# Optimization experiments

Measured on AMD Instinct MI355X. Metric: run time of the kernel, lower is better.

## Reference

```python
import jax, jax.numpy as jnp
import numpy as np

DIM = 2048
N_HEADS = 32
N_KV_HEADS = 8
HEAD_DIM = 64
BATCH = 2
SEQ = 2048
N_REP = N_HEADS // N_KV_HEADS
SCALE = HEAD_DIM ** -0.5
ROPE_BASE = 10000.0


def setup_inputs() -> dict:
    key = jax.random.key(0)
    ks = jax.random.split(key, 5)
    x = jax.random.normal(ks[0], (BATCH, SEQ, DIM), dtype=jnp.float32)
    # weights stored as (in, out) so projection is x @ W
    Wq = jax.random.normal(ks[1], (DIM, N_HEADS * HEAD_DIM), dtype=jnp.float32) * (DIM ** -0.5)
    Wk = jax.random.normal(ks[2], (DIM, N_KV_HEADS * HEAD_DIM), dtype=jnp.float32) * (DIM ** -0.5)
    Wv = jax.random.normal(ks[3], (DIM, N_KV_HEADS * HEAD_DIM), dtype=jnp.float32) * (DIM ** -0.5)
    Wo = jax.random.normal(ks[4], (N_HEADS * HEAD_DIM, DIM), dtype=jnp.float32) * ((N_HEADS * HEAD_DIM) ** -0.5)
    # RoPE tables (seq, head_dim)
    inv_freq = 1.0 / (ROPE_BASE ** (jnp.arange(0, HEAD_DIM, 2, dtype=jnp.float32) / HEAD_DIM))
    t = jnp.arange(SEQ, dtype=jnp.float32)
    freqs = jnp.outer(t, inv_freq)                      # (S, D/2)
    emb = jnp.concatenate([freqs, freqs], axis=-1)      # (S, D)
    cos = jnp.cos(emb)
    sin = jnp.sin(emb)
    # additive causal mask (1,1,S,S)
    neg = jnp.finfo(jnp.float32).min
    causal = jnp.tril(jnp.ones((SEQ, SEQ), dtype=bool))
    attention_mask = jnp.where(causal, 0.0, neg)[None, None, :, :].astype(jnp.float32)
    return {"x": x, "Wq": Wq, "Wk": Wk, "Wv": Wv, "Wo": Wo,
            "cos": cos, "sin": sin, "attention_mask": attention_mask}


def _rotate_half(u):
    h = u.shape[-1] // 2
    return jnp.concatenate([-u[..., h:], u[..., :h]], axis=-1)


def reference(x, Wq, Wk, Wv, Wo, cos, sin, attention_mask):
    b, s, _ = x.shape
    q = (x @ Wq).reshape(b, s, N_HEADS, HEAD_DIM)
    k = (x @ Wk).reshape(b, s, N_KV_HEADS, HEAD_DIM)
    v = (x @ Wv).reshape(b, s, N_KV_HEADS, HEAD_DIM)
    # RoPE, broadcast over head dim (unsqueeze_dim=2)
    c = cos[None, :, None, :]
    sn = sin[None, :, None, :]
    q = q * c + _rotate_half(q) * sn
    k = k * c + _rotate_half(k) * sn
    # repeat KV heads for GQA: (b,s,kvh,d) -> (b,s,h,d)
    k = jnp.repeat(k, N_REP, axis=2)
    v = jnp.repeat(v, N_REP, axis=2)
    # (b,h,s,d)
    q = q.transpose(0, 2, 1, 3)
    k = k.transpose(0, 2, 1, 3)
    v = v.transpose(0, 2, 1, 3)
    scores = jnp.einsum("bhqd,bhkd->bhqk", q, k) * SCALE + attention_mask
    attn = jax.nn.softmax(scores.astype(jnp.float32), axis=-1).astype(q.dtype)
    out = jnp.einsum("bhqk,bhkd->bhqd", attn, v)
    out = out.transpose(0, 2, 1, 3).reshape(b, s, N_HEADS * HEAD_DIM)
    return out @ Wo
```

## Files before the change

kernel.cpp:

```cpp
#include <hip/hip_runtime.h>
#include <hip/hip_bf16.h>

typedef unsigned short u16;
typedef unsigned int   u32;
typedef __bf16 bf16_t;
typedef bf16_t bf16x8 __attribute__((ext_vector_type(8)));
typedef u16    u16x8  __attribute__((ext_vector_type(8)));
typedef float  f32x4  __attribute__((ext_vector_type(4)));

#define DIM  2048
#define SEQ  2048
#define BATCH 2
#define NH   32
#define NKVH 8
#define HD   64
#define KVDIM (NKVH*HD)
#define NQKV (DIM + 2*KVDIM)
#define SCALE 0.125f

__device__ __forceinline__ float b2f(u16 u) {
  union { u32 i; float f; } v; v.i = ((u32)u) << 16; return v.f;
}
__device__ __forceinline__ u16 f2b(float f) {
  union { float f; u32 i; } v; v.f = f;
  u32 x = v.i;
  return (u16)((x + 0x7fffu + ((x >> 16) & 1u)) >> 16);
}
__device__ __forceinline__ u32 pkbf2(float a, float b) {
  __hip_bfloat162 h = __float22bfloat162_rn(float2{a, b});
  union { __hip_bfloat162 h; u32 u; } v; v.h = h; return v.u;
}
__device__ __forceinline__ int probe_bf16(const u32* probe) { return probe[0] != 0u; }
__device__ __forceinline__ float ext_ld(const void* p, long idx, int mode_bf16) {
  return mode_bf16 ? b2f(((const u16*)p)[idx]) : ((const float*)p)[idx];
}
__device__ __forceinline__ void gload_lds16(const u16* g, u16* l) {
  __builtin_amdgcn_global_load_lds((const __attribute__((address_space(1))) void*)g,
                                   (__attribute__((address_space(3))) void*)l, 16, 0, 0);
}

struct SwapT   { static constexpr bool value = true;  };
struct NoSwapT { static constexpr bool value = false; };

__global__ void cast_x(const void* __restrict__ in, u16* __restrict__ out,
                       const u32* __restrict__ probe) {
  int mode = probe_bf16(probe);
  if (mode) return;
  long base = ((long)blockIdx.x * 256 + threadIdx.x) * 8;
  float4 f0 = *(const float4*)((const float*)in + base);
  float4 f1 = *(const float4*)((const float*)in + base + 4);
  u16x8 t;
  t[0] = f2b(f0.x); t[1] = f2b(f0.y); t[2] = f2b(f0.z); t[3] = f2b(f0.w);
  t[4] = f2b(f1.x); t[5] = f2b(f1.y); t[6] = f2b(f1.z); t[7] = f2b(f1.w);
  *(u16x8*)&out[base] = t;
}

__global__ void transpose_qkv(const void* __restrict__ Wq, const void* __restrict__ Wk,
                              const void* __restrict__ Wv, u16* __restrict__ out,
                              const u32* __restrict__ probe) {
  int mode = probe_bf16(probe);
  __shared__ u16 t[32][33];
  int xt = blockIdx.x;
  const void* in; int C, c0, obase;
  if (xt < 64)      { in = Wq; C = DIM;   c0 = xt * 32;        obase = 0; }
  else if (xt < 80) { in = Wk; C = KVDIM; c0 = (xt - 64) * 32; obase = DIM; }
  else              { in = Wv; C = KVDIM; c0 = (xt - 80) * 32; obase = DIM + KVDIM; }
  int r0 = blockIdx.y * 32;
  int tx = threadIdx.x, ty = threadIdx.y;
#pragma unroll
  for (int i = 0; i < 32; i += 8)
    t[ty + i][tx] = mode ? ((const u16*)in)[(long)(r0 + ty + i) * C + c0 + tx]
                         : f2b(((const float*)in)[(long)(r0 + ty + i) * C + c0 + tx]);
  __syncthreads();
#pragma unroll
  for (int i = 0; i < 32; i += 8)
    out[(long)(obase + c0 + ty + i) * DIM + r0 + tx] = t[tx][ty + i];
}

__global__ void transpose_w(const void* __restrict__ in, u16* __restrict__ out,
                            int R, int C, const u32* __restrict__ probe) {
  int mode = probe_bf16(probe);
  __shared__ u16 t[32][33];
  int c0 = blockIdx.x * 32, r0 = blockIdx.y * 32;
  int tx = threadIdx.x, ty = threadIdx.y;
#pragma unroll
  for (int i = 0; i < 32; i += 8)
    t[ty + i][tx] = mode ? ((const u16*)in)[(long)(r0 + ty + i) * C + c0 + tx]
                         : f2b(((const float*)in)[(long)(r0 + ty + i) * C + c0 + tx]);
  __syncthreads();
#pragma unroll
  for (int i = 0; i < 32; i += 8)
    out[(long)(c0 + ty + i) * R + r0 + tx] = t[tx][ty + i];
}

__global__ void rope_both(u16* __restrict__ Qb, u16* __restrict__ Kb,
                          const void* __restrict__ cosb, const void* __restrict__ sinb,
                          const u32* __restrict__ probe) {
  int mode = probe_bf16(probe);
  long gid = (long)blockIdx.x * 256 + threadIdx.x;
  const long NQp = (long)BATCH * SEQ * NH * 32;
  u16* base_p; int n_heads; long t; float osc;
  if (gid < NQp) { base_p = Qb; n_heads = NH; t = gid; osc = SCALE; }
  else           { base_p = Kb; n_heads = NKVH; t = gid - NQp; osc = 1.0f; }
  int pair = t & 31;
  long t2 = t >> 5;
  int h = (int)(t2 % n_heads);
  long row = t2 / n_heads;
  int s = (int)(row & (SEQ - 1));
  long base = row * (n_heads * HD) + h * HD + pair;
  float q0 = b2f(base_p[base]), q1 = b2f(base_p[base + 32]);
  float c0 = ext_ld(cosb, (long)s * HD + pair, mode);
  float c1 = ext_ld(cosb, (long)s * HD + pair + 32, mode);
  float s0 = ext_ld(sinb, (long)s * HD + pair, mode);
  float s1 = ext_ld(sinb, (long)s * HD + pair + 32, mode);
  base_p[base]      = f2b((q0 * c0 - q1 * s0) * osc);
  base_p[base + 32] = f2b((q1 * c1 + q0 * s1) * osc);
}


__launch_bounds__(256)
__global__ void gemm_qkv(const void* __restrict__ x, const u16* __restrict__ xb,
                         int use_xb, const u16* __restrict__ Bt,
                         u16* __restrict__ Qb, u16* __restrict__ Kb, u16* __restrict__ Vt,
                         const u32* __restrict__ probe) {
  int pmode = probe_bf16(probe);
  int mode = (use_xb || pmode) ? 1 : 0;
  const u16* A16 = pmode ? (const u16*)x : xb;
  const float* Af = (const float*)x;
  __shared__ __align__(16) u16 As[128 * 32];
  __shared__ __align__(16) u16 Bs[128 * 32];
  int tid = threadIdx.x, lane = tid & 63, wv = tid >> 6;
  int l16 = lane & 15, q = lane >> 4;
  int wg = blockIdx.y * 24 + blockIdx.x;
  int xcd = wg & 7, tch = wg >> 3;
  int bm0 = (tch / 3) * 128;
  int bn0 = (xcd * 3 + tch % 3) * 128;
  int mbase = (wv & 1) * 64, nbase = (wv >> 1) * 64;
  int c0 = tid, c1 = tid + 256;
  int r0 = c0 >> 2, s0 = (c0 & 3) ^ ((r0 >> 1) & 3);
  int r1 = c1 >> 2, s1 = (c1 & 3) ^ ((r1 >> 1) & 3);
  const int K = DIM;
  long aoff0 = (long)(bm0 + r0) * K + s0 * 8;
  long aoff1 = (long)(bm0 + r1) * K + s1 * 8;
  long boff0 = (long)(bn0 + r0) * K + s0 * 8;
  long boff1 = (long)(bn0 + r1) * K + s1 * 8;
  int rsw = (q ^ ((l16 >> 1) & 3)) * 8;
  f32x4 acc[4][4] = {};

  auto kloop = [&](auto tag) {
    constexpr bool SWAP = decltype(tag)::value;
    for (int k0 = 0; k0 < K; k0 += 32) {
      __syncthreads();
      if (mode) {
        gload_lds16(A16 + aoff0 + k0, &As[wv * 512]);
        gload_lds16(A16 + aoff1 + k0, &As[2048 + wv * 512]);
      } else {
        float4 f0 = *(const float4*)(Af + aoff0 + k0);
        float4 f1 = *(const float4*)(Af + aoff0 + k0 + 4);
        u16x8 t;
        t[0] = f2b(f0.x); t[1] = f2b(f0.y); t[2] = f2b(f0.z); t[3] = f2b(f0.w);
        t[4] = f2b(f1.x); t[5] = f2b(f1.y); t[6] = f2b(f1.z); t[7] = f2b(f1.w);
        *(u16x8*)&As[c0 * 8] = t;
        float4 g0 = *(const float4*)(Af + aoff1 + k0);
        float4 g1 = *(const float4*)(Af + aoff1 + k0 + 4);
        u16x8 u;
        u[0] = f2b(g0.x); u[1] = f2b(g0.y); u[2] = f2b(g0.z); u[3] = f2b(g0.w);
        u[4] = f2b(g1.x); u[5] = f2b(g1.y); u[6] = f2b(g1.z); u[7] = f2b(g1.w);
        *(u16x8*)&As[c1 * 8] = u;
      }
      gload_lds16(Bt + boff0 + k0, &Bs[wv * 512]);
      gload_lds16(Bt + boff1 + k0, &Bs[2048 + wv * 512]);
      __syncthreads();
      bf16x8 af[4], bfr[4];
#pragma unroll
      for (int mi = 0; mi < 4; mi++)
        af[mi] = *(const bf16x8*)&As[(mbase + mi * 16 + l16) * 32 + rsw];
#pragma unroll
      for (int ni = 0; ni < 4; ni++)
        bfr[ni] = *(const bf16x8*)&Bs[(nbase + ni * 16 + l16) * 32 + rsw];
#pragma unroll
      for (int mi = 0; mi < 4; mi++)
#pragma unroll
        for (int ni = 0; ni < 4; ni++) {
          if constexpr (SWAP)
            acc[mi][ni] = __builtin_amdgcn_mfma_f32_16x16x32_bf16(
                bfr[ni], af[mi], acc[mi][ni], 0, 0, 0);
          else
            acc[mi][ni] = __builtin_amdgcn_mfma_f32_16x16x32_bf16(
                af[mi], bfr[ni], acc[mi][ni], 0, 0, 0);
        }
    }
  };

  if (bn0 < DIM + KVDIM) {
    kloop(SwapT{});
    u16* Cb; int ldc, ncol0;
    if (bn0 < DIM) { Cb = Qb; ldc = DIM; ncol0 = bn0; }
    else           { Cb = Kb; ldc = KVDIM; ncol0 = bn0 - DIM; }
#pragma unroll
    for (int mi = 0; mi < 4; mi++)
#pragma unroll
      for (int ni = 0; ni < 4; ni++) {
        int m = bm0 + mbase + mi * 16 + l16;
        int n0 = ncol0 + nbase + ni * 16 + q * 4;
        uint2 w;
        w.x = pkbf2(acc[mi][ni][0], acc[mi][ni][1]);
        w.y = pkbf2(acc[mi][ni][2], acc[mi][ni][3]);
        *(uint2*)&Cb[(long)m * ldc + n0] = w;
      }
  } else {
    kloop(NoSwapT{});
    int vcol0 = bn0 - DIM - KVDIM;
#pragma unroll
    for (int mi = 0; mi < 4; mi++)
#pragma unroll
      for (int ni = 0; ni < 4; ni++) {
        int vcol = vcol0 + nbase + ni * 16 + l16;
        int kvh2 = vcol >> 6, d = vcol & 63;
        int m = bm0 + mbase + mi * 16 + q * 4;
        int bb = m >> 11, s = m & (SEQ - 1);
        uint2 w;
        w.x = pkbf2(acc[mi][ni][0], acc[mi][ni][1]);
        w.y = pkbf2(acc[mi][ni][2], acc[mi][ni][3]);
        *(uint2*)&Vt[((long)(bb * NKVH + kvh2) * HD + d) * SEQ + s] = w;
      }
  }
}

__launch_bounds__(256)
__global__ void gemm_ao(const u16* __restrict__ A, const u16* __restrict__ Bt,
                        void* __restrict__ C, const u32* __restrict__ probe) {
  int mode = probe_bf16(probe);
  __shared__ __align__(16) u16 As[128 * 32];
  __shared__ __align__(16) u16 Bs[128 * 32];
  int tid = threadIdx.x, lane = tid & 63, wv = tid >> 6;
  int l16 = lane & 15, q = lane >> 4;
  int wg = blockIdx.y * 16 + blockIdx.x;
  int xcd = wg & 7, tch = wg >> 3;
  int bm0 = (tch / 2) * 128;
  int bn0 = (xcd * 2 + tch % 2) * 128;
  int mbase = (wv & 1) * 64, nbase = (wv >> 1) * 64;
  int c0 = tid, c1 = tid + 256;
  int r0 = c0 >> 2, s0 = (c0 & 3) ^ ((r0 >> 1) & 3);
  int r1 = c1 >> 2, s1 = (c1 & 3) ^ ((r1 >> 1) & 3);
  const int K = DIM;
  long aoff0 = (long)(bm0 + r0) * K + s0 * 8;
  long aoff1 = (long)(bm0 + r1) * K + s1 * 8;
  long boff0 = (long)(bn0 + r0) * K + s0 * 8;
  long boff1 = (long)(bn0 + r1) * K + s1 * 8;
  int rsw = (q ^ ((l16 >> 1) & 3)) * 8;
  f32x4 acc[4][4] = {};
  for (int k0 = 0; k0 < K; k0 += 32) {
    __syncthreads();
    gload_lds16(A + aoff0 + k0, &As[wv * 512]);
    gload_lds16(A + aoff1 + k0, &As[2048 + wv * 512]);
    gload_lds16(Bt + boff0 + k0, &Bs[wv * 512]);
    gload_lds16(Bt + boff1 + k0, &Bs[2048 + wv * 512]);
    __syncthreads();
    bf16x8 af[4], bfr[4];
#pragma unroll
    for (int mi = 0; mi < 4; mi++)
      af[mi] = *(const bf16x8*)&As[(mbase + mi * 16 + l16) * 32 + rsw];
#pragma unroll
    for (int ni = 0; ni < 4; ni++)
      bfr[ni] = *(const bf16x8*)&Bs[(nbase + ni * 16 + l16) * 32 + rsw];
#pragma unroll
    for (int mi = 0; mi < 4; mi++)
#pragma unroll
      for (int ni = 0; ni < 4; ni++)
        acc[mi][ni] = __builtin_amdgcn_mfma_f32_16x16x32_bf16(
            bfr[ni], af[mi], acc[mi][ni], 0, 0, 0);
  }
#pragma unroll
  for (int mi = 0; mi < 4; mi++)
#pragma unroll
    for (int ni = 0; ni < 4; ni++) {
      int m = bm0 + mbase + mi * 16 + l16;
      int n0 = bn0 + nbase + ni * 16 + q * 4;
      if (mode) {
        uint2 w;
        w.x = pkbf2(acc[mi][ni][0], acc[mi][ni][1]);
        w.y = pkbf2(acc[mi][ni][2], acc[mi][ni][3]);
        *(uint2*)&((u16*)C)[(long)m * DIM + n0] = w;
      } else {
        float4 f;
        f.x = acc[mi][ni][0]; f.y = acc[mi][ni][1];
        f.z = acc[mi][ni][2]; f.w = acc[mi][ni][3];
        *(float4*)&((float*)C)[(long)m * DIM + n0] = f;
      }
    }
}

__launch_bounds__(256, 4)
__global__ void attn_kernel(const u16* __restrict__ Q, const u16* __restrict__ K,
                            const u16* __restrict__ Vt, u16* __restrict__ AO) {
  __shared__ __align__(16) u16 Ks[2 * 64 * 64];
  __shared__ __align__(16) u16 Vs[2 * 64 * 64];
  __shared__ __align__(16) u16 Ps[4][16 * 64];
  int tid = threadIdx.x, lane = tid & 63, wv = tid >> 6;
  int l16 = lane & 15, q = lane >> 4;
  int i = blockIdx.x;
  int bh = blockIdx.y;
  int b = bh >> 5, h = bh & 31, kvh = h >> 2;
  const u16* Kp = K + (long)b * SEQ * KVDIM + kvh * HD;
  const u16* Vp = Vt + (long)(b * NKVH + kvh) * HD * SEQ;

  int cA = tid, cB = tid + 256;
  int rA = cA >> 3, bA = (cA & 7) ^ (rA & 7);
  int rB = cB >> 3, bB = (cB & 7) ^ (rB & 7);
  const u16* kSrcA = Kp + (long)rA * KVDIM + bA * 8;
  const u16* kSrcB = Kp + (long)rB * KVDIM + bB * 8;
  const u16* vSrcA = Vp + (long)rA * SEQ + bA * 8;
  const u16* vSrcB = Vp + (long)rB * SEQ + bB * 8;
  u16* kDstA = &Ks[(wv * 64 + lane) * 8];
  u16* kDstB = &Ks[(256 + wv * 64 + lane) * 8];
  u16* vDstA = &Vs[(wv * 64 + lane) * 8];
  u16* vDstB = &Vs[(256 + wv * 64 + lane) * 8];

  int e = l16 & 7;
  int off0 = (q ^ e) * 8;
  int off1 = ((4 + q) ^ e) * 8;

  bf16x8 ones;
#pragma unroll
  for (int j = 0; j < 8; j++) ones[j] = (bf16_t)1.0f;

#pragma unroll
  for (int ph = 0; ph < 2; ph++) {
    int t = ph ? (31 - i) : i;
    int qbase = t * 64 + wv * 16;
    const u16* Qp = Q + (long)(b * SEQ + qbase) * DIM + h * HD;
    bf16x8 aq0 = *(const bf16x8*)&Qp[l16 * DIM + q * 8];
    bf16x8 aq1 = *(const bf16x8*)&Qp[l16 * DIM + 32 + q * 8];
    f32x4 o_acc[4] = {};
    f32x4 l_acc = {};
    int qrow = qbase + l16;

    __syncthreads();
    gload_lds16(kSrcA, kDstA);
    gload_lds16(kSrcB, kDstB);
    gload_lds16(vSrcA, vDstA);
    gload_lds16(vSrcB, vDstB);
    int curo = 0;

    for (int kt = 0; kt <= t; kt++) {
      __syncthreads();
      if (kt < t) {
        long kk2 = (long)(kt + 1) * 64;
        int nxt = curo ^ 4096;
        gload_lds16(kSrcA + kk2 * KVDIM, kDstA + nxt);
        gload_lds16(kSrcB + kk2 * KVDIM, kDstB + nxt);
        gload_lds16(vSrcA + kk2, vDstA + nxt);
        gload_lds16(vSrcB + kk2, vDstB + nxt);
      }
      const u16* Ksb = &Ks[curo];
      const u16* Vsb = &Vs[curo];
      long kk = (long)kt * 64;

      f32x4 sc[4];
#pragma unroll
      for (int ni = 0; ni < 4; ni++) {
        bf16x8 bk0 = *(const bf16x8*)&Ksb[(ni * 16 + l16) * 64 + off0];
        bf16x8 bk1 = *(const bf16x8*)&Ksb[(ni * 16 + l16) * 64 + off1];
        f32x4 z = {};
        z = __builtin_amdgcn_mfma_f32_16x16x32_bf16(bk0, aq0, z, 0, 0, 0);
        z = __builtin_amdgcn_mfma_f32_16x16x32_bf16(bk1, aq1, z, 0, 0, 0);
        sc[ni] = z;
      }
      if (kt == t) {
#pragma unroll
        for (int ni = 0; ni < 4; ni++)
#pragma unroll
          for (int r = 0; r < 4; r++) {
            int kv = (int)kk + ni * 16 + q * 4 + r;
            float p = __expf(sc[ni][r]);
            sc[ni][r] = (kv <= qrow) ? p : 0.f;
          }
      } else {
#pragma unroll
        for (int ni = 0; ni < 4; ni++)
#pragma unroll
          for (int r = 0; r < 4; r++) sc[ni][r] = __expf(sc[ni][r]);
      }
#pragma unroll
      for (int ni = 0; ni < 4; ni++) {
        uint2 w;
        w.x = pkbf2(sc[ni][0], sc[ni][1]);
        w.y = pkbf2(sc[ni][2], sc[ni][3]);
        int pblk = (2 * ni + (q >> 1)) ^ e;
        *(uint2*)&Ps[wv][l16 * 64 + pblk * 8 + (q & 1) * 4] = w;
      }
      bf16x8 ap0 = *(const bf16x8*)&Ps[wv][l16 * 64 + off0];
      bf16x8 ap1 = *(const bf16x8*)&Ps[wv][l16 * 64 + off1];
      l_acc = __builtin_amdgcn_mfma_f32_16x16x32_bf16(ap0, ones, l_acc, 0, 0, 0);
      l_acc = __builtin_amdgcn_mfma_f32_16x16x32_bf16(ap1, ones, l_acc, 0, 0, 0);
#pragma unroll
      for (int di = 0; di < 4; di++) {
        bf16x8 bv0 = *(const bf16x8*)&Vsb[(di * 16 + l16) * 64 + off0];
        bf16x8 bv1 = *(const bf16x8*)&Vsb[(di * 16 + l16) * 64 + off1];
        o_acc[di] = __builtin_amdgcn_mfma_f32_16x16x32_bf16(ap0, bv0, o_acc[di], 0, 0, 0);
        o_acc[di] = __builtin_amdgcn_mfma_f32_16x16x32_bf16(ap1, bv1, o_acc[di], 0, 0, 0);
      }
      curo ^= 4096;
    }
    long obase = (long)(b * SEQ + qbase + q * 4) * DIM + h * HD;
#pragma unroll
    for (int r = 0; r < 4; r++) {
      float inv = 1.0f / l_acc[r];
#pragma unroll
      for (int di = 0; di < 4; di++)
        AO[obase + (long)r * DIM + di * 16 + l16] = f2b(o_acc[di][r] * inv);
    }
  }
}

extern "C" void kernel_launch(void* const* d_in, const int* in_sizes, int n_in,
                              void* d_out, int out_size, void* d_ws, size_t ws_size,
                              hipStream_t stream) {
  const void* x    = d_in[0];
  const void* Wq   = d_in[1];
  const void* Wk   = d_in[2];
  const void* Wv   = d_in[3];
  const void* Wo   = d_in[4];
  const void* cosb = d_in[5];
  const void* sinb = d_in[6];
  const u32*  probe = (const u32*)d_in[7];

  u16* WqkvT = (u16*)d_ws;
  u16* WoT = WqkvT + (size_t)NQKV * DIM;
  u16* Qb  = WoT + (size_t)DIM * DIM;
  u16* Kb  = Qb  + (size_t)BATCH * SEQ * DIM;
  u16* Vt  = Kb  + (size_t)BATCH * SEQ * KVDIM;
  u16* xb  = Vt  + (size_t)BATCH * NKVH * HD * SEQ;
  u16* AO  = Qb;

  size_t need_xb = ((size_t)(xb - WqkvT) + (size_t)BATCH * SEQ * DIM) * sizeof(u16);
  int use_xb = ws_size >= need_xb;

  dim3 blk32(32, 8);
  transpose_qkv<<<dim3(96, 64), blk32, 0, stream>>>(Wq, Wk, Wv, WqkvT, probe);
  transpose_w<<<dim3(DIM / 32, DIM / 32), blk32, 0, stream>>>(Wo, WoT, DIM, DIM, probe);

  int M = BATCH * SEQ;
  if (use_xb) {
    cast_x<<<(M * DIM) / (256 * 8), 256, 0, stream>>>(x, xb, probe);
    gemm_qkv<<<dim3(NQKV / 128, M / 128), 256, 0, stream>>>(x, xb, 1, WqkvT, Qb, Kb, Vt, probe);
  } else {
    gemm_qkv<<<dim3(NQKV / 128, M / 128), 256, 0, stream>>>(x, nullptr, 0, WqkvT, Qb, Kb, Vt, probe);
  }

  long rope_slots = (long)M * NH * 32 + (long)M * NKVH * 32;
  rope_both<<<(int)(rope_slots / 256), 256, 0, stream>>>(Qb, Kb, cosb, sinb, probe);

  attn_kernel<<<dim3(16, BATCH * NH), 256, 0, stream>>>(Qb, Kb, Vt, AO);

  gemm_ao<<<dim3(DIM / 128, M / 128), 256, 0, stream>>>(AO, WoT, d_out, probe);
}
```

Measured before the change: 331.1 us.

## Merge prep kernels, drop XCD swizzle, and double attention query tile per wave

Fuses the weight transposes and the x cast into one prep launch, which cuts kernel launch overhead. Removes the XCD-aware tile remapping in both GEMMs and uses plain block indexing. Reworks attention so each wave handles 32 query rows instead of 16, reusing each K/V tile loaded from shared memory across two query sub-tiles, and halves the grid. The cost is higher register pressure (launch bounds lowered to 2), fewer blocks, and possible loss of L2 locality from dropping the swizzle.

```diff
diff --git a/kernel.cpp b/kernel.cpp
--- a/kernel.cpp
+++ b/kernel.cpp
@@ -42,55 +42,41 @@
 struct SwapT   { static constexpr bool value = true;  };
 struct NoSwapT { static constexpr bool value = false; };
 
-__global__ void cast_x(const void* __restrict__ in, u16* __restrict__ out,
-                       const u32* __restrict__ probe) {
+__global__ void prep(const void* __restrict__ Wq, const void* __restrict__ Wk,
+                     const void* __restrict__ Wv, const void* __restrict__ Wo,
+                     const void* __restrict__ x, u16* __restrict__ WqkvT,
+                     u16* __restrict__ WoT, u16* __restrict__ xb, int use_xb,
+                     const u32* __restrict__ probe) {
   int mode = probe_bf16(probe);
-  if (mode) return;
-  long base = ((long)blockIdx.x * 256 + threadIdx.x) * 8;
-  float4 f0 = *(const float4*)((const float*)in + base);
-  float4 f1 = *(const float4*)((const float*)in + base + 4);
-  u16x8 t;
-  t[0] = f2b(f0.x); t[1] = f2b(f0.y); t[2] = f2b(f0.z); t[3] = f2b(f0.w);
-  t[4] = f2b(f1.x); t[5] = f2b(f1.y); t[6] = f2b(f1.z); t[7] = f2b(f1.w);
-  *(u16x8*)&out[base] = t;
-}
-
-__global__ void transpose_qkv(const void* __restrict__ Wq, const void* __restrict__ Wk,
-                              const void* __restrict__ Wv, u16* __restrict__ out,
-                              const u32* __restrict__ probe) {
-  int mode = probe_bf16(probe);
-  __shared__ u16 t[32][33];
   int xt = blockIdx.x;
-  const void* in; int C, c0, obase;
-  if (xt < 64)      { in = Wq; C = DIM;   c0 = xt * 32;        obase = 0; }
-  else if (xt < 80) { in = Wk; C = KVDIM; c0 = (xt - 64) * 32; obase = DIM; }
-  else              { in = Wv; C = KVDIM; c0 = (xt - 80) * 32; obase = DIM + KVDIM; }
-  int r0 = blockIdx.y * 32;
   int tx = threadIdx.x, ty = threadIdx.y;
-#pragma unroll
-  for (int i = 0; i < 32; i += 8)
-    t[ty + i][tx] = mode ? ((const u16*)in)[(long)(r0 + ty + i) * C + c0 + tx]
-                         : f2b(((const float*)in)[(long)(r0 + ty + i) * C + c0 + tx]);
-  __syncthreads();
-#pragma unroll
-  for (int i = 0; i < 32; i += 8)
-    out[(long)(obase + c0 + ty + i) * DIM + r0 + tx] = t[tx][ty + i];
-}
-
-__global__ void transpose_w(const void* __restrict__ in, u16* __restrict__ out,
-                            int R, int C, const u32* __restrict__ probe) {
-  int mode = probe_bf16(probe);
-  __shared__ u16 t[32][33];
-  int c0 = blockIdx.x * 32, r0 = blockIdx.y * 32;
-  int tx = threadIdx.x, ty = threadIdx.y;
-#pragma unroll
-  for (int i = 0; i < 32; i += 8)
-    t[ty + i][tx] = mode ? ((const u16*)in)[(long)(r0 + ty + i) * C + c0 + tx]
-                         : f2b(((const float*)in)[(long)(r0 + ty + i) * C + c0 + tx]);
-  __syncthreads();
-#pragma unroll
-  for (int i = 0; i < 32; i += 8)
-    out[(long)(c0 + ty + i) * R + r0 + tx] = t[tx][ty + i];
+  if (xt < 160) {
+    __shared__ u16 t[32][33];
+    const void* in; int C, c0, obase; u16* out; int ld;
+    if (xt < 64)       { in = Wq; C = DIM;   c0 = xt * 32;        obase = 0;           out = WqkvT; ld = DIM; }
+    else if (xt < 80)  { in = Wk; C = KVDIM; c0 = (xt - 64) * 32; obase = DIM;         out = WqkvT; ld = DIM; }
+    else if (xt < 96)  { in = Wv; C = KVDIM; c0 = (xt - 80) * 32; obase = DIM + KVDIM; out = WqkvT; ld = DIM; }
+    else               { in = Wo; C = DIM;   c0 = (xt - 96) * 32; obase = 0;           out = WoT;   ld = DIM; }
+    int r0 = blockIdx.y * 32;
+#pragma unroll
+    for (int i = 0; i < 32; i += 8)
+      t[ty + i][tx] = mode ? ((const u16*)in)[(long)(r0 + ty + i) * C + c0 + tx]
+                           : f2b(((const float*)in)[(long)(r0 + ty + i) * C + c0 + tx]);
+    __syncthreads();
+#pragma unroll
+    for (int i = 0; i < 32; i += 8)
+      out[(long)(obase + c0 + ty + i) * ld + r0 + tx] = t[tx][ty + i];
+  } else {
+    if (mode || !use_xb) return;
+    int tid = ty * 32 + tx;
+    long base = ((long)((xt - 160) * 64 + blockIdx.y) * 256 + tid) * 8;
+    float4 f0 = *(const float4*)((const float*)x + base);
+    float4 f1 = *(const float4*)((const float*)x + base + 4);
+    u16x8 t8;
+    t8[0] = f2b(f0.x); t8[1] = f2b(f0.y); t8[2] = f2b(f0.z); t8[3] = f2b(f0.w);
+    t8[4] = f2b(f1.x); t8[5] = f2b(f1.y); t8[6] = f2b(f1.z); t8[7] = f2b(f1.w);
+    *(u16x8*)&xb[base] = t8;
+  }
 }
 
 __global__ void rope_both(u16* __restrict__ Qb, u16* __restrict__ Kb,
@@ -131,10 +117,7 @@
   __shared__ __align__(16) u16 Bs[128 * 32];
   int tid = threadIdx.x, lane = tid & 63, wv = tid >> 6;
   int l16 = lane & 15, q = lane >> 4;
-  int wg = blockIdx.y * 24 + blockIdx.x;
-  int xcd = wg & 7, tch = wg >> 3;
-  int bm0 = (tch / 3) * 128;
-  int bn0 = (xcd * 3 + tch % 3) * 128;
+  int bm0 = blockIdx.y * 128, bn0 = blockIdx.x * 128;
   int mbase = (wv & 1) * 64, nbase = (wv >> 1) * 64;
   int c0 = tid, c1 = tid + 256;
   int r0 = c0 >> 2, s0 = (c0 & 3) ^ ((r0 >> 1) & 3);
@@ -235,10 +218,7 @@
   __shared__ __align__(16) u16 Bs[128 * 32];
   int tid = threadIdx.x, lane = tid & 63, wv = tid >> 6;
   int l16 = lane & 15, q = lane >> 4;
-  int wg = blockIdx.y * 16 + blockIdx.x;
-  int xcd = wg & 7, tch = wg >> 3;
-  int bm0 = (tch / 2) * 128;
-  int bn0 = (xcd * 2 + tch % 2) * 128;
+  int bm0 = blockIdx.y * 128, bn0 = blockIdx.x * 128;
   int mbase = (wv & 1) * 64, nbase = (wv >> 1) * 64;
   int c0 = tid, c1 = tid + 256;
   int r0 = c0 >> 2, s0 = (c0 & 3) ^ ((r0 >> 1) & 3);
@@ -291,12 +271,12 @@
     }
 }
 
-__launch_bounds__(256, 4)
+__launch_bounds__(256, 2)
 __global__ void attn_kernel(const u16* __restrict__ Q, const u16* __restrict__ K,
                             const u16* __restrict__ Vt, u16* __restrict__ AO) {
   __shared__ __align__(16) u16 Ks[2 * 64 * 64];
   __shared__ __align__(16) u16 Vs[2 * 64 * 64];
-  __shared__ __align__(16) u16 Ps[4][16 * 64];
+  __shared__ __align__(16) u16 Ps[4][32 * 64];
   int tid = threadIdx.x, lane = tid & 63, wv = tid >> 6;
   int l16 = lane & 15, q = lane >> 4;
   int i = blockIdx.x;
@@ -327,14 +307,19 @@
 
 #pragma unroll
   for (int ph = 0; ph < 2; ph++) {
-    int t = ph ? (31 - i) : i;
-    int qbase = t * 64 + wv * 16;
+    int t = ph ? (15 - i) : i;
+    int qbase = t * 128 + wv * 32;
     const u16* Qp = Q + (long)(b * SEQ + qbase) * DIM + h * HD;
-    bf16x8 aq0 = *(const bf16x8*)&Qp[l16 * DIM + q * 8];
-    bf16x8 aq1 = *(const bf16x8*)&Qp[l16 * DIM + 32 + q * 8];
-    f32x4 o_acc[4] = {};
-    f32x4 l_acc = {};
-    int qrow = qbase + l16;
+    bf16x8 aq[2][2];
+#pragma unroll
+    for (int qr = 0; qr < 2; qr++) {
+      aq[qr][0] = *(const bf16x8*)&Qp[(qr * 16 + l16) * DIM + q * 8];
+      aq[qr][1] = *(const bf16x8*)&Qp[(qr * 16 + l16) * DIM + 32 + q * 8];
+    }
+    f32x4 o_acc[2][4] = {};
+    f32x4 l_acc[2] = {};
+    int nkt = 2 * (t + 1);
+    int wmax = qbase + 31;
 
     __syncthreads();
     gload_lds16(kSrcA, kDstA);
@@ -343,9 +328,9 @@
     gload_lds16(vSrcB, vDstB);
     int curo = 0;
 
-    for (int kt = 0; kt <= t; kt++) {
+    for (int kt = 0; kt < nkt; kt++) {
       __syncthreads();
-      if (kt < t) {
+      if (kt + 1 < nkt) {
         long kk2 = (long)(kt + 1) * 64;
         int nxt = curo ^ 4096;
         gload_lds16(kSrcA + kk2 * KVDIM, kDstA + nxt);
@@ -353,63 +338,81 @@
         gload_lds16(vSrcA + kk2, vDstA + nxt);
         gload_lds16(vSrcB + kk2, vDstB + nxt);
       }
+      int kk = kt * 64;
+      if (kk > wmax) { curo ^= 4096; continue; }
       const u16* Ksb = &Ks[curo];
       const u16* Vsb = &Vs[curo];
-      long kk = (long)kt * 64;
-
-      f32x4 sc[4];
+
+      bf16x8 bk[4][2], bv[4][2];
 #pragma unroll
       for (int ni = 0; ni < 4; ni++) {
-        bf16x8 bk0 = *(const bf16x8*)&Ksb[(ni * 16 + l16) * 64 + off0];
-        bf16x8 bk1 = *(const bf16x8*)&Ksb[(ni * 16 + l16) * 64 + off1];
-        f32x4 z = {};
-        z = __builtin_amdgcn_mfma_f32_16x16x32_bf16(bk0, aq0, z, 0, 0, 0);
-        z = __builtin_amdgcn_mfma_f32_16x16x32_bf16(bk1, aq1, z, 0, 0, 0);
-        sc[ni] = z;
-      }
-      if (kt == t) {
-#pragma unroll
-        for (int ni = 0; ni < 4; ni++)
-#pragma unroll
-          for (int r = 0; r < 4; r++) {
-            int kv = (int)kk + ni * 16 + q * 4 + r;
-            float p = __expf(sc[ni][r]);
-            sc[ni][r] = (kv <= qrow) ? p : 0.f;
-          }
-      } else {
-#pragma unroll
-        for (int ni = 0; ni < 4; ni++)
-#pragma unroll
-          for (int r = 0; r < 4; r++) sc[ni][r] = __expf(sc[ni][r]);
-      }
-#pragma unroll
-      for (int ni = 0; ni < 4; ni++) {
-        uint2 w;
-        w.x = pkbf2(sc[ni][0], sc[ni][1]);
-        w.y = pkbf2(sc[ni][2], sc[ni][3]);
-        int pblk = (2 * ni + (q >> 1)) ^ e;
-        *(uint2*)&Ps[wv][l16 * 64 + pblk * 8 + (q & 1) * 4] = w;
-      }
-      bf16x8 ap0 = *(const bf16x8*)&Ps[wv][l16 * 64 + off0];
-      bf16x8 ap1 = *(const bf16x8*)&Ps[wv][l16 * 64 + off1];
-      l_acc = __builtin_amdgcn_mfma_f32_16x16x32_bf16(ap0, ones, l_acc, 0, 0, 0);
-      l_acc = __builtin_amdgcn_mfma_f32_16x16x32_bf16(ap1, ones, l_acc, 0, 0, 0);
+        bk[ni][0] = *(const bf16x8*)&Ksb[(ni * 16 + l16) * 64 + off0];
+        bk[ni][1] = *(const bf16x8*)&Ksb[(ni * 16 + l16) * 64 + off1];
+      }
 #pragma unroll
       for (int di = 0; di < 4; di++) {
-        bf16x8 bv0 = *(const bf16x8*)&Vsb[(di * 16 + l16) * 64 + off0];
-        bf16x8 bv1 = *(const bf16x8*)&Vsb[(di * 16 + l16) * 64 + off1];
-        o_acc[di] = __builtin_amdgcn_mfma_f32_16x16x32_bf16(ap0, bv0, o_acc[di], 0, 0, 0);
-        o_acc[di] = __builtin_amdgcn_mfma_f32_16x16x32_bf16(ap1, bv1, o_acc[di], 0, 0, 0);
+        bv[di][0] = *(const bf16x8*)&Vsb[(di * 16 + l16) * 64 + off0];
+        bv[di][1] = *(const bf16x8*)&Vsb[(di * 16 + l16) * 64 + off1];
+      }
+      bool diag = (kt >= 2 * t);
+#pragma unroll
+      for (int qr = 0; qr < 2; qr++) {
+        int qb16 = qbase + qr * 16;
+        if (kk > qb16 + 15) continue;
+        f32x4 sc[4];
+#pragma unroll
+        for (int ni = 0; ni < 4; ni++) {
+          f32x4 z = {};
+          z = __builtin_amdgcn_mfma_f32_16x16x32_bf16(bk[ni][0], aq[qr][0], z, 0, 0, 0);
+          z = __builtin_amdgcn_mfma_f32_16x16x32_bf16(bk[ni][1], aq[qr][1], z, 0, 0, 0);
+          sc[ni] = z;
+        }
+        int qrow = qb16 + l16;
+        if (diag) {
+#pragma unroll
+          for (int ni = 0; ni < 4; ni++)
+#pragma unroll
+            for (int r = 0; r < 4; r++) {
+              int kv = kk + ni * 16 + q * 4 + r;
+              float p = __expf(sc[ni][r]);
+              sc[ni][r] = (kv <= qrow) ? p : 0.f;
+            }
+        } else {
+#pragma unroll
+          for (int ni = 0; ni < 4; ni++)
+#pragma unroll
+            for (int r = 0; r < 4; r++) sc[ni][r] = __expf(sc[ni][r]);
+        }
+#pragma unroll
+        for (int ni = 0; ni < 4; ni++) {
+          uint2 w;
+          w.x = pkbf2(sc[ni][0], sc[ni][1]);
+          w.y = pkbf2(sc[ni][2], sc[ni][3]);
+          int pblk = (2 * ni + (q >> 1)) ^ e;
+          *(uint2*)&Ps[wv][(qr * 16 + l16) * 64 + pblk * 8 + (q & 1) * 4] = w;
+        }
+        bf16x8 ap0 = *(const bf16x8*)&Ps[wv][(qr * 16 + l16) * 64 + off0];
+        bf16x8 ap1 = *(const bf16x8*)&Ps[wv][(qr * 16 + l16) * 64 + off1];
+        l_acc[qr] = __builtin_amdgcn_mfma_f32_16x16x32_bf16(ap0, ones, l_acc[qr], 0, 0, 0);
+        l_acc[qr] = __builtin_amdgcn_mfma_f32_16x16x32_bf16(ap1, ones, l_acc[qr], 0, 0, 0);
+#pragma unroll
+        for (int di = 0; di < 4; di++) {
+          o_acc[qr][di] = __builtin_amdgcn_mfma_f32_16x16x32_bf16(ap0, bv[di][0], o_acc[qr][di], 0, 0, 0);
+          o_acc[qr][di] = __builtin_amdgcn_mfma_f32_16x16x32_bf16(ap1, bv[di][1], o_acc[qr][di], 0, 0, 0);
+        }
       }
       curo ^= 4096;
     }
-    long obase = (long)(b * SEQ + qbase + q * 4) * DIM + h * HD;
-#pragma unroll
-    for (int r = 0; r < 4; r++) {
-      float inv = 1.0f / l_acc[r];
-#pragma unroll
-      for (int di = 0; di < 4; di++)
-        AO[obase + (long)r * DIM + di * 16 + l16] = f2b(o_acc[di][r] * inv);
+#pragma unroll
+    for (int qr = 0; qr < 2; qr++) {
+      long obase = (long)(b * SEQ + qbase + qr * 16 + q * 4) * DIM + h * HD;
+#pragma unroll
+      for (int r = 0; r < 4; r++) {
+        float inv = 1.0f / l_acc[qr][r];
+#pragma unroll
+        for (int di = 0; di < 4; di++)
+          AO[obase + (long)r * DIM + di * 16 + l16] = f2b(o_acc[qr][di][r] * inv);
+      }
     }
   }
 }
@@ -437,22 +440,16 @@
   size_t need_xb = ((size_t)(xb - WqkvT) + (size_t)BATCH * SEQ * DIM) * sizeof(u16);
   int use_xb = ws_size >= need_xb;
 
-  dim3 blk32(32, 8);
-  transpose_qkv<<<dim3(96, 64), blk32, 0, stream>>>(Wq, Wk, Wv, WqkvT, probe);
-  transpose_w<<<dim3(DIM / 32, DIM / 32), blk32, 0, stream>>>(Wo, WoT, DIM, DIM, probe);
-
   int M = BATCH * SEQ;
-  if (use_xb) {
-    cast_x<<<(M * DIM) / (256 * 8), 256, 0, stream>>>(x, xb, probe);
-    gemm_qkv<<<dim3(NQKV / 128, M / 128), 256, 0, stream>>>(x, xb, 1, WqkvT, Qb, Kb, Vt, probe);
-  } else {
-    gemm_qkv<<<dim3(NQKV / 128, M / 128), 256, 0, stream>>>(x, nullptr, 0, WqkvT, Qb, Kb, Vt, probe);
-  }
+  prep<<<dim3(224, 64), dim3(32, 8), 0, stream>>>(Wq, Wk, Wv, Wo, x, WqkvT, WoT,
+                                                  xb, use_xb, probe);
+  gemm_qkv<<<dim3(NQKV / 128, M / 128), 256, 0, stream>>>(x, xb, use_xb, WqkvT,
+                                                          Qb, Kb, Vt, probe);
 
   long rope_slots = (long)M * NH * 32 + (long)M * NKVH * 32;
   rope_both<<<(int)(rope_slots / 256), 256, 0, stream>>>(Qb, Kb, cosb, sinb, probe);
 
-  attn_kernel<<<dim3(16, BATCH * NH), 256, 0, stream>>>(Qb, Kb, Vt, AO);
+  attn_kernel<<<dim3(8, BATCH * NH), 256, 0, stream>>>(Qb, Kb, Vt, AO);
 
   gemm_ao<<<dim3(DIM / 128, M / 128), 256, 0, stream>>>(AO, WoT, d_out, probe);
 }
```

Measured after the change: 332.0 us. Within noise of the previous version (+0.3%).
